# Performance work log

Hardware: AMD Instinct MI355X
Metric: run time of the kernel (lower is better)

Reference implementation:

```python
import jax, jax.numpy as jnp
import numpy as np

N_E = 1024     # codebook size (n_e, nbooks=1)
E_DIM = 256    # embedding dim
BETA = 0.25
B, T = 16, 4096


def setup_inputs() -> dict:
    key = jax.random.key(0)
    k1, k2 = jax.random.split(key)
    z = jax.random.normal(k1, (B, T, E_DIM), dtype=jnp.float32)
    # matches torch init: uniform(-1/n_e_i, 1/n_e_i)
    codebook = jax.random.uniform(k2, (N_E, E_DIM), dtype=jnp.float32,
                                  minval=-1.0 / N_E, maxval=1.0 / N_E)
    return {"z": z, "codebook": codebook}


def reference(z, codebook):
    zf = z.reshape(-1, E_DIM)                                   # [N, d]
    dist = (jnp.sum(zf * zf, axis=1, keepdims=True)
            - 2.0 * (zf @ codebook.T)
            + jnp.sum(codebook * codebook, axis=1)[None, :])
    idx = jnp.argmin(dist, axis=1)                              # [N]
    # one-hot scatter + matmul == codebook gather
    z_q = codebook[idx].reshape(z.shape)                        # [B, T, d]
    loss = (jnp.mean((z_q - jax.lax.stop_gradient(z)) ** 2)
            + BETA * jnp.mean((z - jax.lax.stop_gradient(z_q)) ** 2))
    # straight-through estimator
    z_q_st = z + jax.lax.stop_gradient(z_q - z)
    indices = idx.reshape(z.shape[:-1] + (1,))                  # [B, T, 1]
    return z_q_st, loss, indices
```

## Files before the change

kernel.cpp:

```cpp
#include <hip/hip_runtime.h>
#include <hip/hip_bf16.h>
#include <math.h>

typedef __bf16 bf16x8 __attribute__((ext_vector_type(8)));
typedef float f32x4 __attribute__((ext_vector_type(4)));
typedef unsigned short u16x8 __attribute__((ext_vector_type(8)));

constexpr int EDIM = 256;
constexpr int NE = 1024;
constexpr int NROWS = 65536;
constexpr float BETA = 0.25f;

constexpr size_t B2T_OFF   = 0;
constexpr size_t B2T_SZ    = (size_t)8 * 16 * 8192;
constexpr size_t SZROW_OFF = B2T_OFF + B2T_SZ;
constexpr size_t SZABS_OFF = SZROW_OFF + 262144;
constexpr size_t CNORM_OFF = SZABS_OFF + 262144;
constexpr size_t EMAX_OFF  = CNORM_OFF + 4096;
constexpr size_t CNT_OFF   = EMAX_OFF + 256;
constexpr size_t LIST_OFF  = CNT_OFF + 256;
constexpr size_t LPART_OFF = LIST_OFF + 262144;
constexpr size_t LP2_OFF   = LPART_OFF + 262144;
constexpr size_t WS_NEED   = LP2_OFF + 1024;

__device__ __forceinline__ unsigned short f32_to_bf16_rne(float f) {
    unsigned u = __float_as_uint(f);
    u += 0x7fffu + ((u >> 16) & 1u);
    return (unsigned short)(u >> 16);
}
__device__ __forceinline__ float bf16_to_f32(unsigned short h) {
    return __uint_as_float((unsigned)h << 16);
}

#define GLL16(g, l)                                                                   \
    __builtin_amdgcn_global_load_lds(                                                 \
        (const __attribute__((address_space(1))) unsigned int*)(g),                   \
        (__attribute__((address_space(3))) unsigned int*)(l), 16, 0, 0)

__global__ __launch_bounds__(64)
void p3_codebook(const float* __restrict__ cb, float* __restrict__ cnorm,
                 char* __restrict__ B2t, unsigned* __restrict__ emax_u) {
    __shared__ float xr[256];
    __shared__ float rres[16];
    __shared__ unsigned short ehi[256], elo[256];
    const int e = blockIdx.x, l = threadIdx.x;
    const float4 v = reinterpret_cast<const float4*>(cb + (size_t)e * EDIM)[l];
    *reinterpret_cast<float4*>(&xr[l * 4]) = v;
    float amax = fmaxf(fmaxf(fabsf(v.x), fabsf(v.y)), fmaxf(fabsf(v.z), fabsf(v.w)));
    #pragma unroll
    for (int off = 32; off; off >>= 1) amax = fmaxf(amax, __shfl_down(amax, off));
    __syncthreads();
    #pragma unroll
    for (int i = 0; i < 4; ++i) {
        const int idx = i * 64 + l;
        const float f = xr[idx];
        const unsigned short h = f32_to_bf16_rne(f);
        ehi[idx] = h;
        elo[idx] = f32_to_bf16_rne(f - bf16_to_f32(h));
    }
    if (l < 16) {
        const float* x = xr + (l >> 3) * 128;
        const int j = l & 7;
        float r = __fmul_rn(x[j], x[j]);
        for (int i = 8; i < 128; i += 8) r = __fadd_rn(r, __fmul_rn(x[i + j], x[i + j]));
        rres[l] = r;
    }
    __syncthreads();
    if (l == 0) {
        float h0 = __fadd_rn(__fadd_rn(__fadd_rn(rres[0], rres[1]), __fadd_rn(rres[2], rres[3])),
                             __fadd_rn(__fadd_rn(rres[4], rres[5]), __fadd_rn(rres[6], rres[7])));
        float h1 = __fadd_rn(__fadd_rn(__fadd_rn(rres[8], rres[9]), __fadd_rn(rres[10], rres[11])),
                             __fadd_rn(__fadd_rn(rres[12], rres[13]), __fadd_rn(rres[14], rres[15])));
        cnorm[e] = __fadd_rn(h0, h1);
        atomicMax(emax_u, __float_as_uint(amax));
    }
    {
        const int c = l >> 2, kgv = l & 3;
        const int colbase = ((c < 8) ? c * 32 : (c - 8) * 32) + kgv * 8;
        const unsigned short* src = (c < 8) ? ehi : elo;
        char* dst = B2t + ((((size_t)(e >> 7) * 16 + c) * 512 + (size_t)kgv * 128 + (e & 127)) * 16);
        *reinterpret_cast<uint4*>(dst) = *reinterpret_cast<const uint4*>(&src[colbase]);
    }
}

__global__ __launch_bounds__(256, 2)
void vq_main(const float* __restrict__ z, const char* __restrict__ B2t,
             const float* __restrict__ cnorm, const float* __restrict__ emaxp,
             const float* __restrict__ cb,
             float* __restrict__ idxf, int* __restrict__ cnt, int* __restrict__ list,
             float* __restrict__ zq, float* __restrict__ lpart,
             float* __restrict__ szrow, float* __restrict__ szabs) {
    constexpr int CNS = 65536;
    __shared__ char smem[71680] __attribute__((aligned(16)));
    float* cns  = reinterpret_cast<float*>(smem + CNS);
    float* szsr = reinterpret_cast<float*>(smem + 70656);
    float* szsa = reinterpret_cast<float*>(smem + 70912);
    float (*ms1)[2] = reinterpret_cast<float(*)[2]>(smem);
    float (*ms2)[2] = reinterpret_cast<float(*)[2]>(smem + 512);
    int   (*mi1)[2] = reinterpret_cast<int(*)[2]>(smem + 1024);
    int*  bidx      = reinterpret_cast<int*>(smem + 1536);

    const int tid = threadIdx.x;
    const int mtile = blockIdx.x;
    const size_t rowbase = (size_t)mtile * 64;
    const int l = tid & 63, wid = tid >> 6;
    const int kg = l >> 4, li = l & 15;
    const int wr = wid >> 1, wc = wid & 1;

    {
        float* t = reinterpret_cast<float*>(smem);
        #pragma unroll
        for (int i = 0; i < 16; ++i) {
            const int fid = i * 256 + tid;
            const int r = fid >> 6, c4 = fid & 63;
            const float4 v = *reinterpret_cast<const float4*>(
                z + (rowbase + r) * EDIM + c4 * 4);
            *reinterpret_cast<float4*>(&t[r * 260 + c4 * 4]) = v;
        }
    }
    __syncthreads();
    {
        float* t = reinterpret_cast<float*>(smem);
        float (*ch)[16] = reinterpret_cast<float(*)[16]>(smem + 66560);
        const int r = tid >> 2, q = tid & 3;
        float asum = 0.f;
        for (int c = 0; c < 64; ++c) asum += fabsf(t[r * 260 + q * 64 + c]);
        asum += __shfl_xor(asum, 1);
        asum += __shfl_xor(asum, 2);
        #pragma unroll
        for (int cc = 0; cc < 4; ++cc) {
            const int chain = q * 4 + cc;
            const float* x = &t[r * 260 + (chain >> 3) * 128];
            const int j = chain & 7;
            float rr = __fmul_rn(x[j], x[j]);
            for (int i = 8; i < 128; i += 8) rr = __fadd_rn(rr, __fmul_rn(x[i + j], x[i + j]));
            ch[r][chain] = rr;
        }
        __syncthreads();
        if (q == 0) {
            const float* c0 = ch[r];
            const float h0 = __fadd_rn(__fadd_rn(__fadd_rn(c0[0], c0[1]), __fadd_rn(c0[2], c0[3])),
                                       __fadd_rn(__fadd_rn(c0[4], c0[5]), __fadd_rn(c0[6], c0[7])));
            const float h1 = __fadd_rn(__fadd_rn(__fadd_rn(c0[8], c0[9]), __fadd_rn(c0[10], c0[11])),
                                       __fadd_rn(__fadd_rn(c0[12], c0[13]), __fadd_rn(c0[14], c0[15])));
            const float sz = __fadd_rn(h0, h1);
            szsr[r] = sz; szsa[r] = asum;
            szrow[rowbase + r] = sz;
            szabs[rowbase + r] = asum;
        }
    }
    u16x8 chi[8], clo[8];
    {
        float* t = reinterpret_cast<float*>(smem);
        const int r = tid >> 2, q = tid & 3;
        #pragma unroll
        for (int s = 0; s < 8; ++s) {
            u16x8 h, lw;
            #pragma unroll
            for (int j = 0; j < 8; ++j) {
                const float f = t[r * 260 + q * 64 + s * 8 + j];
                const unsigned short hh = f32_to_bf16_rne(f);
                h[j] = hh;
                lw[j] = f32_to_bf16_rne(f - bf16_to_f32(hh));
            }
            chi[s] = h; clo[s] = lw;
        }
    }
    __syncthreads();
    {
        const int r = tid >> 2, q = tid & 3;
        #pragma unroll
        for (int s = 0; s < 8; ++s) {
            const int ca = 2 * q + (s >> 2), kgv = s & 3;
            *reinterpret_cast<u16x8*>(smem + (ca * 256 + kgv * 64 + r) * 16) = chi[s];
            *reinterpret_cast<u16x8*>(smem + ((8 + ca) * 256 + kgv * 64 + r) * 16) = clo[s];
        }
    }
    GLL16((const char*)cnorm + tid * 16, smem + CNS + tid * 16);
    asm volatile("s_waitcnt vmcnt(0)" ::: "memory");
    __syncthreads();

    int aoff[2], boff[4];
    #pragma unroll
    for (int f = 0; f < 2; ++f)
        aoff[f] = kg * 1024 + (wr * 32 + f * 16 + li) * 16;
    #pragma unroll
    for (int f = 0; f < 4; ++f)
        boff[f] = kg * 2048 + (wc * 64 + f * 16 + li) * 16;

    bf16x8 cAh[2], cAl[2], cB[4];
    #pragma unroll
    for (int f = 0; f < 2; ++f) {
        cAh[f] = *reinterpret_cast<const bf16x8*>(smem + 0 * 4096 + aoff[f]);
        cAl[f] = *reinterpret_cast<const bf16x8*>(smem + 8 * 4096 + aoff[f]);
    }
    #pragma unroll
    for (int f = 0; f < 4; ++f)
        cB[f] = *reinterpret_cast<const bf16x8*>(B2t + boff[f]);

    float s1v[2][4], s2v[2][4];
    int i1v[2][4];
    #pragma unroll
    for (int a = 0; a < 2; ++a)
        #pragma unroll
        for (int b = 0; b < 4; ++b) { s1v[a][b] = 3.4e38f; s2v[a][b] = 3.4e38f; i1v[a][b] = 0; }

    for (int nt = 0; nt < 8; ++nt) {
        f32x4 acc[2][4];
        const f32x4 zf4 = {0.f, 0.f, 0.f, 0.f};
        #pragma unroll
        for (int a = 0; a < 2; ++a)
            #pragma unroll
            for (int b = 0; b < 4; ++b) acc[a][b] = zf4;

        #pragma unroll
        for (int j = 0; j < 16; ++j) {
            const int g = nt * 16 + j;
            bf16x8 nAh[2], nAl[2], nB[4];
            {
                const int jn = (j + 1) & 15;
                const char* gB = B2t + (size_t)(g + 1) * 8192;
                #pragma unroll
                for (int f = 0; f < 4; ++f)
                    nB[f] = *reinterpret_cast<const bf16x8*>(gB + boff[f]);
                if (jn < 8) {
                    #pragma unroll
                    for (int f = 0; f < 2; ++f) {
                        nAh[f] = *reinterpret_cast<const bf16x8*>(smem + jn * 4096 + aoff[f]);
                        nAl[f] = *reinterpret_cast<const bf16x8*>(smem + (8 + jn) * 4096 + aoff[f]);
                    }
                } else {
                    #pragma unroll
                    for (int f = 0; f < 2; ++f) {
                        nAh[f] = *reinterpret_cast<const bf16x8*>(smem + (jn - 8) * 4096 + aoff[f]);
                        nAl[f] = cAl[f];
                    }
                }
            }
            #pragma unroll
            for (int fm = 0; fm < 2; ++fm)
                #pragma unroll
                for (int fn = 0; fn < 4; ++fn)
                    acc[fm][fn] = __builtin_amdgcn_mfma_f32_16x16x32_bf16(cAh[fm], cB[fn], acc[fm][fn], 0, 0, 0);
            if (j < 8) {
                #pragma unroll
                for (int fm = 0; fm < 2; ++fm)
                    #pragma unroll
                    for (int fn = 0; fn < 4; ++fn)
                        acc[fm][fn] = __builtin_amdgcn_mfma_f32_16x16x32_bf16(cAl[fm], cB[fn], acc[fm][fn], 0, 0, 0);
            }
            #pragma unroll
            for (int f = 0; f < 2; ++f) { cAh[f] = nAh[f]; cAl[f] = nAl[f]; }
            #pragma unroll
            for (int f = 0; f < 4; ++f) cB[f] = nB[f];
        }

        const int ntb = nt * 128;
        #pragma unroll
        for (int fn = 0; fn < 4; ++fn) {
            const int e = ntb + wc * 64 + fn * 16 + li;
            const float cn = cns[e];
            #pragma unroll
            for (int fm = 0; fm < 2; ++fm)
                #pragma unroll
                for (int r = 0; r < 4; ++r) {
                    const float s = cn - 2.0f * acc[fm][fn][r];
                    if (s < s1v[fm][r]) { s2v[fm][r] = s1v[fm][r]; s1v[fm][r] = s; i1v[fm][r] = e; }
                    else s2v[fm][r] = fminf(s2v[fm][r], s);
                }
        }
    }

    __syncthreads();

    #pragma unroll
    for (int fm = 0; fm < 2; ++fm)
        #pragma unroll
        for (int r = 0; r < 4; ++r) {
            float s1 = s1v[fm][r], s2 = s2v[fm][r];
            int i1 = i1v[fm][r];
            #pragma unroll
            for (int off = 1; off < 16; off <<= 1) {
                const float os1 = __shfl_xor(s1, off);
                const float os2 = __shfl_xor(s2, off);
                const int oi1 = __shfl_xor(i1, off);
                const bool take = (os1 < s1) || (os1 == s1 && oi1 < i1);
                const float loser = take ? s1 : os1;
                if (take) { s1 = os1; i1 = oi1; }
                s2 = fminf(fminf(s2, os2), loser);
            }
            if (li == 0) {
                const int rloc = wr * 32 + fm * 16 + (kg << 2) + r;
                ms1[rloc][wc] = s1; ms2[rloc][wc] = s2; mi1[rloc][wc] = i1;
            }
        }
    __syncthreads();

    if (tid < 64) {
        const float a1 = ms1[tid][0], b1 = ms1[tid][1];
        const float a2 = ms2[tid][0], b2 = ms2[tid][1];
        const int ai = mi1[tid][0], bi = mi1[tid][1];
        const bool take = (b1 < a1) || (b1 == a1 && bi < ai);
        const float s1 = take ? b1 : a1;
        const int i1 = take ? bi : ai;
        const float loser = take ? a1 : b1;
        const float s2 = fminf(fminf(a2, b2), loser);
        const int rowg = (int)rowbase + tid;
        const float szv = szsr[tid], sab = szsa[tid];
        const float M = 2.0e-4f * sab * emaxp[0] + ldexpf(1.0f, ilogbf(szv * 1.02f) - 23);
        idxf[rowg] = (float)i1;
        lpart[rowg] = s1 + szv;
        bidx[tid] = i1;
        if (s2 - s1 <= 2.0f * M) { const int p = atomicAdd(cnt, 1); list[p] = rowg; }
    }
    __syncthreads();

    {
        const float4* cb4 = reinterpret_cast<const float4*>(cb);
        float4* zq4 = reinterpret_cast<float4*>(zq);
        #pragma unroll 4
        for (int j = 0; j < 16; ++j) {
            const int rr = wid * 16 + j;
            const int e = bidx[rr];
            zq4[(rowbase + rr) * 64 + l] = cb4[(size_t)e * 64 + l];
        }
    }
}

__global__ __launch_bounds__(256)
void vq_rescan(const float* __restrict__ z, const float* __restrict__ cb,
               const float* __restrict__ cnorm, const float* __restrict__ szrow,
               const int* __restrict__ list, const int* __restrict__ cntp,
               float* __restrict__ idxf, float* __restrict__ zq, float* __restrict__ lpart) {
    __shared__ float zr[8][260];
    __shared__ float szs[8];
    __shared__ int rows_s[8];
    __shared__ float sred[256];
    __shared__ int ired[256];
    const int tid = threadIdx.x;
    const int n = cntp[0];
    const int groups = (n + 7) >> 3;
    for (int g = blockIdx.x; g < groups; g += gridDim.x) {
        if (tid < 8) {
            const int gi = g * 8 + tid;
            const int row = (gi < n) ? list[gi] : -1;
            rows_s[tid] = row;
            szs[tid] = (row >= 0) ? szrow[row] : 0.f;
        }
        __syncthreads();
        #pragma unroll
        for (int i = 0; i < 8; ++i) {
            const int sid = i * 256 + tid;
            const int rr = sid >> 8, k = sid & 255;
            if (rows_s[rr] >= 0) zr[rr][k] = z[(size_t)rows_s[rr] * EDIM + k];
        }
        __syncthreads();
        float bs[8];
        int bi[8];
        #pragma unroll
        for (int rr = 0; rr < 8; ++rr) { bs[rr] = 3.4e38f; bi[rr] = 0; }
        for (int q = 0; q < 4; ++q) {
            const int e = tid + q * 256;
            const float4* crow = reinterpret_cast<const float4*>(cb + (size_t)e * EDIM);
            float d[8];
            #pragma unroll
            for (int rr = 0; rr < 8; ++rr) d[rr] = 0.f;
            for (int k4 = 0; k4 < 64; ++k4) {
                const float4 c4 = crow[k4];
                #pragma unroll
                for (int rr = 0; rr < 8; ++rr) {
                    d[rr] = fmaf(zr[rr][k4 * 4 + 0], c4.x, d[rr]);
                    d[rr] = fmaf(zr[rr][k4 * 4 + 1], c4.y, d[rr]);
                    d[rr] = fmaf(zr[rr][k4 * 4 + 2], c4.z, d[rr]);
                    d[rr] = fmaf(zr[rr][k4 * 4 + 3], c4.w, d[rr]);
                }
            }
            const float cn = cnorm[e];
            #pragma unroll
            for (int rr = 0; rr < 8; ++rr) {
                const float b1 = __fadd_rn(szs[rr], __fmul_rn(-2.0f, d[rr]));
                const float s = __fadd_rn(b1, cn);
                if (s < bs[rr]) { bs[rr] = s; bi[rr] = e; }
            }
        }
        #pragma unroll
        for (int rr = 0; rr < 8; ++rr) {
            sred[tid] = bs[rr];
            ired[tid] = bi[rr];
            __syncthreads();
            for (int h = 128; h; h >>= 1) {
                if (tid < h) {
                    const float so = sred[tid + h];
                    const int io = ired[tid + h];
                    if (so < sred[tid] || (so == sred[tid] && io < ired[tid])) {
                        sred[tid] = so; ired[tid] = io;
                    }
                }
                __syncthreads();
            }
            if (rows_s[rr] >= 0) {
                const int best = ired[0];
                const int row = rows_s[rr];
                zq[(size_t)row * EDIM + tid] = cb[(size_t)best * EDIM + tid];
                if (tid == 0) { idxf[row] = (float)best; lpart[row] = sred[0]; }
            }
            __syncthreads();
        }
    }
}

__global__ void vq_loss1(const float* __restrict__ lpart, float* __restrict__ lp2) {
    __shared__ float red[256];
    const int t = threadIdx.x;
    red[t] = lpart[blockIdx.x * 256 + t];
    __syncthreads();
    for (int h = 128; h; h >>= 1) {
        if (t < h) red[t] += red[t + h];
        __syncthreads();
    }
    if (t == 0) lp2[blockIdx.x] = red[0];
}
__global__ void vq_loss2(const float* __restrict__ lp2, float* __restrict__ outloss) {
    __shared__ float red[256];
    const int t = threadIdx.x;
    red[t] = lp2[t];
    __syncthreads();
    for (int h = 128; h; h >>= 1) {
        if (t < h) red[t] += red[t + h];
        __syncthreads();
    }
    if (t == 0) outloss[0] = red[0] * ((1.0f + BETA) / 16777216.0f);
}

__device__ __forceinline__ float np_sum128_sq(const float* __restrict__ x) {
    float r[8];
    #pragma unroll
    for (int j = 0; j < 8; ++j) r[j] = __fmul_rn(x[j], x[j]);
    #pragma unroll
    for (int i = 8; i < 128; i += 8)
        #pragma unroll
        for (int j = 0; j < 8; ++j) r[j] = __fadd_rn(r[j], __fmul_rn(x[i + j], x[i + j]));
    return __fadd_rn(__fadd_rn(__fadd_rn(r[0], r[1]), __fadd_rn(r[2], r[3])),
                     __fadd_rn(__fadd_rn(r[4], r[5]), __fadd_rn(r[6], r[7])));
}
__global__ void fb_prep(const float* __restrict__ z, const float* __restrict__ cb,
                        float* __restrict__ szrow, float* __restrict__ cnorm) {
    int t = blockIdx.x * blockDim.x + threadIdx.x;
    if (t < NROWS) {
        const float* x = z + (size_t)t * EDIM;
        szrow[t] = __fadd_rn(np_sum128_sq(x), np_sum128_sq(x + 128));
    } else if (t < NROWS + NE) {
        const float* x = cb + (size_t)(t - NROWS) * EDIM;
        cnorm[t - NROWS] = __fadd_rn(np_sum128_sq(x), np_sum128_sq(x + 128));
    }
}
__global__ __launch_bounds__(256, 2)
void fb_vq(const float* __restrict__ z, const float* __restrict__ cb,
           const float* __restrict__ cnorm, const float* __restrict__ szrow,
           float* __restrict__ zq, float* __restrict__ idxf, float* __restrict__ lpart) {
    __shared__ float As[64 * 268];
    __shared__ float Bs[32 * 68];
    __shared__ int bidx[64];
    __shared__ float lred[4];
    const int tid = threadIdx.x;
    const int tx = tid & 15, ty = tid >> 4;
    const size_t rowbase = (size_t)blockIdx.x * 64;
    const float4* zg = reinterpret_cast<const float4*>(z + rowbase * EDIM);
    #pragma unroll
    for (int it = 0; it < 16; ++it) {
        int id = it * 256 + tid;
        int r = id >> 6, c4 = id & 63;
        float4 v = zg[id];
        *reinterpret_cast<float4*>(&As[r * 268 + c4 * 4]) = v;
    }
    float sz[4];
    #pragma unroll
    for (int m = 0; m < 4; ++m) sz[m] = szrow[rowbase + ty * 4 + m];
    float bestS[4]; int bestI[4];
    #pragma unroll
    for (int m = 0; m < 4; ++m) { bestS[m] = 3.4e38f; bestI[m] = 0; }
    for (int nt = 0; nt < NE / 64; ++nt) {
        float acc[4][4];
        #pragma unroll
        for (int m = 0; m < 4; ++m)
            #pragma unroll
            for (int n = 0; n < 4; ++n) acc[m][n] = 0.f;
        const int ebase = nt * 64;
        for (int k0 = 0; k0 < EDIM; k0 += 32) {
            __syncthreads();
            #pragma unroll
            for (int i = 0; i < 8; ++i) {
                int id = i * 256 + tid;
                int n = id >> 5, k = id & 31;
                Bs[k * 68 + n] = cb[(size_t)(ebase + n) * EDIM + k0 + k];
            }
            __syncthreads();
            #pragma unroll
            for (int kg2 = 0; kg2 < 32; kg2 += 4) {
                float4 a[4], b[4];
                #pragma unroll
                for (int m = 0; m < 4; ++m)
                    a[m] = *reinterpret_cast<const float4*>(&As[(ty * 4 + m) * 268 + k0 + kg2]);
                #pragma unroll
                for (int kk = 0; kk < 4; ++kk)
                    b[kk] = *reinterpret_cast<const float4*>(&Bs[(kg2 + kk) * 68 + tx * 4]);
                #pragma unroll
                for (int m = 0; m < 4; ++m) {
                    const float* av = reinterpret_cast<const float*>(&a[m]);
                    #pragma unroll
                    for (int kk = 0; kk < 4; ++kk) {
                        acc[m][0] = fmaf(av[kk], b[kk].x, acc[m][0]);
                        acc[m][1] = fmaf(av[kk], b[kk].y, acc[m][1]);
                        acc[m][2] = fmaf(av[kk], b[kk].z, acc[m][2]);
                        acc[m][3] = fmaf(av[kk], b[kk].w, acc[m][3]);
                    }
                }
            }
        }
        #pragma unroll
        for (int n = 0; n < 4; ++n) {
            int e = ebase + tx * 4 + n;
            float cn = cnorm[e];
            #pragma unroll
            for (int m = 0; m < 4; ++m) {
                float b1 = __fadd_rn(sz[m], __fmul_rn(-2.0f, acc[m][n]));
                float s = __fadd_rn(b1, cn);
                if (s < bestS[m]) { bestS[m] = s; bestI[m] = e; }
            }
        }
    }
    #pragma unroll
    for (int m = 0; m < 4; ++m) {
        float s = bestS[m]; int i = bestI[m];
        #pragma unroll
        for (int off = 1; off < 16; off <<= 1) {
            float s2 = __shfl_xor(s, off);
            int i2 = __shfl_xor(i, off);
            if (s2 < s || (s2 == s && i2 < i)) { s = s2; i = i2; }
        }
        if (tx == 0) bidx[ty * 4 + m] = i;
    }
    __syncthreads();
    if (tid < 64) idxf[rowbase + tid] = (float)bidx[tid];
    float lsum = 0.f;
    for (int r = 0; r < 64; ++r) {
        int e = bidx[r];
        float c = cb[(size_t)e * EDIM + tid];
        float zv = As[r * 268 + tid];
        float d = c - zv;
        lsum = fmaf(d, d, lsum);
        zq[(rowbase + r) * EDIM + tid] = c;
    }
    #pragma unroll
    for (int off = 32; off; off >>= 1) lsum += __shfl_down(lsum, off);
    if ((tid & 63) == 0) lred[tid >> 6] = lsum;
    __syncthreads();
    if (tid == 0) lpart[blockIdx.x] = lred[0] + lred[1] + lred[2] + lred[3];
}
__global__ void fb_loss(const float* __restrict__ lpart, float* __restrict__ out_loss) {
    __shared__ float red[256];
    int tid = threadIdx.x;
    float s = 0.f;
    for (int i = tid; i < NROWS / 64; i += 256) s += lpart[i];
    red[tid] = s;
    __syncthreads();
    for (int h = 128; h; h >>= 1) {
        if (tid < h) red[tid] += red[tid + h];
        __syncthreads();
    }
    if (tid == 0) out_loss[0] = red[0] * (1.0f + BETA) / (float)((size_t)NROWS * EDIM);
}

extern "C" void kernel_launch(void* const* d_in, const int* in_sizes, int n_in,
                              void* d_out, int out_size, void* d_ws, size_t ws_size,
                              hipStream_t stream) {
    const float* z = (const float*)d_in[0];
    const float* cb = (const float*)d_in[1];
    float* out = (float*)d_out;
    float* zq = out;
    float* loss = out + (size_t)NROWS * EDIM;
    float* idxf = loss + 1;
    char* ws = (char*)d_ws;

    if (ws_size < WS_NEED) {
        float* cnorm = (float*)ws;
        float* szrow = cnorm + NE;
        float* lpart = szrow + NROWS;
        hipLaunchKernelGGL(fb_prep, dim3((NROWS + NE + 255) / 256), dim3(256), 0, stream, z, cb, szrow, cnorm);
        hipLaunchKernelGGL(fb_vq, dim3(NROWS / 64), dim3(256), 0, stream, z, cb, cnorm, szrow, zq, idxf, lpart);
        hipLaunchKernelGGL(fb_loss, dim3(1), dim3(256), 0, stream, lpart, loss);
        return;
    }

    char* B2t = ws + B2T_OFF;
    float* szrow = (float*)(ws + SZROW_OFF);
    float* szabs = (float*)(ws + SZABS_OFF);
    float* cnorm = (float*)(ws + CNORM_OFF);
    float* emax = (float*)(ws + EMAX_OFF);
    int* cnt = (int*)(ws + CNT_OFF);
    int* list = (int*)(ws + LIST_OFF);
    float* lpart = (float*)(ws + LPART_OFF);
    float* lp2 = (float*)(ws + LP2_OFF);

    hipMemsetAsync(emax, 0, 4, stream);
    hipMemsetAsync(cnt, 0, 4, stream);
    hipLaunchKernelGGL(p3_codebook, dim3(NE), dim3(64), 0, stream, cb, cnorm, B2t, (unsigned*)emax);
    hipLaunchKernelGGL(vq_main, dim3(1024), dim3(256), 0, stream,
                       z, B2t, cnorm, emax, cb, idxf, cnt, list, zq, lpart, szrow, szabs);
    hipLaunchKernelGGL(vq_rescan, dim3(1024), dim3(256), 0, stream,
                       z, cb, cnorm, szrow, list, cnt, idxf, zq, lpart);
    hipLaunchKernelGGL(vq_loss1, dim3(256), dim3(256), 0, stream, lpart, lp2);
    hipLaunchKernelGGL(vq_loss2, dim3(1), dim3(256), 0, stream, lp2, loss);
}
```

Measured before the change: 237.5 us.

## Shrink vq_main tile to 32 rows for higher occupancy

Halves the per-block row tile from 64 to 32 rows, so shared memory drops from about 70KB to about 37KB and launch bounds rise to 4 blocks per CU. The grid doubles to 2048 blocks and the four waves now split the 128-code N tile as 1x4 instead of 2x2, with a 4-way cross-wave argmin merge. The goal is more resident waves to hide latency, at the cost of each block streaming the whole bf16 codebook for only half as many rows, which doubles codebook traffic per row.

```diff
diff --git a/kernel.cpp b/kernel.cpp
--- a/kernel.cpp
+++ b/kernel.cpp
@@ -83,34 +83,34 @@
     }
 }
 
-__global__ __launch_bounds__(256, 2)
+__global__ __launch_bounds__(256, 4)
 void vq_main(const float* __restrict__ z, const char* __restrict__ B2t,
              const float* __restrict__ cnorm, const float* __restrict__ emaxp,
              const float* __restrict__ cb,
              float* __restrict__ idxf, int* __restrict__ cnt, int* __restrict__ list,
              float* __restrict__ zq, float* __restrict__ lpart,
              float* __restrict__ szrow, float* __restrict__ szabs) {
-    constexpr int CNS = 65536;
-    __shared__ char smem[71680] __attribute__((aligned(16)));
+    constexpr int CNS = 32768;
+    __shared__ char smem[37120] __attribute__((aligned(16)));
     float* cns  = reinterpret_cast<float*>(smem + CNS);
-    float* szsr = reinterpret_cast<float*>(smem + 70656);
-    float* szsa = reinterpret_cast<float*>(smem + 70912);
-    float (*ms1)[2] = reinterpret_cast<float(*)[2]>(smem);
-    float (*ms2)[2] = reinterpret_cast<float(*)[2]>(smem + 512);
-    int   (*mi1)[2] = reinterpret_cast<int(*)[2]>(smem + 1024);
+    float* szsr = reinterpret_cast<float*>(smem + 36864);
+    float* szsa = reinterpret_cast<float*>(smem + 36992);
+    float (*ms1)[4] = reinterpret_cast<float(*)[4]>(smem);
+    float (*ms2)[4] = reinterpret_cast<float(*)[4]>(smem + 512);
+    int   (*mi1)[4] = reinterpret_cast<int(*)[4]>(smem + 1024);
     int*  bidx      = reinterpret_cast<int*>(smem + 1536);
 
     const int tid = threadIdx.x;
     const int mtile = blockIdx.x;
-    const size_t rowbase = (size_t)mtile * 64;
+    const size_t rowbase = (size_t)mtile * 32;
     const int l = tid & 63, wid = tid >> 6;
     const int kg = l >> 4, li = l & 15;
-    const int wr = wid >> 1, wc = wid & 1;
+    const int wc = wid;
 
     {
         float* t = reinterpret_cast<float*>(smem);
         #pragma unroll
-        for (int i = 0; i < 16; ++i) {
+        for (int i = 0; i < 8; ++i) {
             const int fid = i * 256 + tid;
             const int r = fid >> 6, c4 = fid & 63;
             const float4 v = *reinterpret_cast<const float4*>(
@@ -121,15 +121,16 @@
     __syncthreads();
     {
         float* t = reinterpret_cast<float*>(smem);
-        float (*ch)[16] = reinterpret_cast<float(*)[16]>(smem + 66560);
-        const int r = tid >> 2, q = tid & 3;
+        float (*ch)[16] = reinterpret_cast<float(*)[16]>(smem + 33280);
+        const int r = tid >> 3, q = tid & 7;
         float asum = 0.f;
-        for (int c = 0; c < 64; ++c) asum += fabsf(t[r * 260 + q * 64 + c]);
+        for (int c = 0; c < 32; ++c) asum += fabsf(t[r * 260 + q * 32 + c]);
         asum += __shfl_xor(asum, 1);
         asum += __shfl_xor(asum, 2);
-        #pragma unroll
-        for (int cc = 0; cc < 4; ++cc) {
-            const int chain = q * 4 + cc;
+        asum += __shfl_xor(asum, 4);
+        #pragma unroll
+        for (int cc = 0; cc < 2; ++cc) {
+            const int chain = q * 2 + cc;
             const float* x = &t[r * 260 + (chain >> 3) * 128];
             const int j = chain & 7;
             float rr = __fmul_rn(x[j], x[j]);
@@ -149,16 +150,16 @@
             szabs[rowbase + r] = asum;
         }
     }
-    u16x8 chi[8], clo[8];
+    u16x8 chi[4], clo[4];
     {
         float* t = reinterpret_cast<float*>(smem);
-        const int r = tid >> 2, q = tid & 3;
-        #pragma unroll
-        for (int s = 0; s < 8; ++s) {
+        const int r = tid >> 3, q = tid & 7;
+        #pragma unroll
+        for (int s = 0; s < 4; ++s) {
             u16x8 h, lw;
             #pragma unroll
             for (int j = 0; j < 8; ++j) {
-                const float f = t[r * 260 + q * 64 + s * 8 + j];
+                const float f = t[r * 260 + q * 32 + s * 8 + j];
                 const unsigned short hh = f32_to_bf16_rne(f);
                 h[j] = hh;
                 lw[j] = f32_to_bf16_rne(f - bf16_to_f32(hh));
@@ -168,35 +169,31 @@
     }
     __syncthreads();
     {
-        const int r = tid >> 2, q = tid & 3;
-        #pragma unroll
-        for (int s = 0; s < 8; ++s) {
-            const int ca = 2 * q + (s >> 2), kgv = s & 3;
-            *reinterpret_cast<u16x8*>(smem + (ca * 256 + kgv * 64 + r) * 16) = chi[s];
-            *reinterpret_cast<u16x8*>(smem + ((8 + ca) * 256 + kgv * 64 + r) * 16) = clo[s];
+        const int r = tid >> 3, q = tid & 7;
+        #pragma unroll
+        for (int s = 0; s < 4; ++s) {
+            *reinterpret_cast<u16x8*>(smem + (q * 128 + s * 32 + r) * 16) = chi[s];
+            *reinterpret_cast<u16x8*>(smem + ((8 + q) * 128 + s * 32 + r) * 16) = clo[s];
         }
     }
     GLL16((const char*)cnorm + tid * 16, smem + CNS + tid * 16);
     asm volatile("s_waitcnt vmcnt(0)" ::: "memory");
     __syncthreads();
 
-    int aoff[2], boff[4];
-    #pragma unroll
-    for (int f = 0; f < 2; ++f)
-        aoff[f] = kg * 1024 + (wr * 32 + f * 16 + li) * 16;
-    #pragma unroll
-    for (int f = 0; f < 4; ++f)
-        boff[f] = kg * 2048 + (wc * 64 + f * 16 + li) * 16;
-
-    bf16x8 cAh[2], cAl[2], cB[4];
+    int aoff[2], boff[2];
     #pragma unroll
     for (int f = 0; f < 2; ++f) {
-        cAh[f] = *reinterpret_cast<const bf16x8*>(smem + 0 * 4096 + aoff[f]);
-        cAl[f] = *reinterpret_cast<const bf16x8*>(smem + 8 * 4096 + aoff[f]);
-    }
-    #pragma unroll
-    for (int f = 0; f < 4; ++f)
-        cB[f] = *reinterpret_cast<const bf16x8*>(B2t + boff[f]);
+        aoff[f] = kg * 512 + (f * 16 + li) * 16;
+        boff[f] = kg * 2048 + (wc * 32 + f * 16 + li) * 16;
+    }
+
+    bf16x8 cAh[2], cAl[2], cB[2];
+    #pragma unroll
+    for (int f = 0; f < 2; ++f) {
+        cAh[f] = *reinterpret_cast<const bf16x8*>(smem + 0 * 2048 + aoff[f]);
+        cAl[f] = *reinterpret_cast<const bf16x8*>(smem + 8 * 2048 + aoff[f]);
+        cB[f]  = *reinterpret_cast<const bf16x8*>(B2t + boff[f]);
+    }
 
     float s1v[2][4], s2v[2][4];
     int i1v[2][4];
@@ -206,33 +203,33 @@
         for (int b = 0; b < 4; ++b) { s1v[a][b] = 3.4e38f; s2v[a][b] = 3.4e38f; i1v[a][b] = 0; }
 
     for (int nt = 0; nt < 8; ++nt) {
-        f32x4 acc[2][4];
+        f32x4 acc[2][2];
         const f32x4 zf4 = {0.f, 0.f, 0.f, 0.f};
         #pragma unroll
         for (int a = 0; a < 2; ++a)
             #pragma unroll
-            for (int b = 0; b < 4; ++b) acc[a][b] = zf4;
+            for (int b = 0; b < 2; ++b) acc[a][b] = zf4;
 
         #pragma unroll
         for (int j = 0; j < 16; ++j) {
             const int g = nt * 16 + j;
-            bf16x8 nAh[2], nAl[2], nB[4];
+            bf16x8 nAh[2], nAl[2], nB[2];
             {
                 const int jn = (j + 1) & 15;
                 const char* gB = B2t + (size_t)(g + 1) * 8192;
                 #pragma unroll
-                for (int f = 0; f < 4; ++f)
+                for (int f = 0; f < 2; ++f)
                     nB[f] = *reinterpret_cast<const bf16x8*>(gB + boff[f]);
                 if (jn < 8) {
                     #pragma unroll
                     for (int f = 0; f < 2; ++f) {
-                        nAh[f] = *reinterpret_cast<const bf16x8*>(smem + jn * 4096 + aoff[f]);
-                        nAl[f] = *reinterpret_cast<const bf16x8*>(smem + (8 + jn) * 4096 + aoff[f]);
+                        nAh[f] = *reinterpret_cast<const bf16x8*>(smem + jn * 2048 + aoff[f]);
+                        nAl[f] = *reinterpret_cast<const bf16x8*>(smem + (8 + jn) * 2048 + aoff[f]);
                     }
                 } else {
                     #pragma unroll
                     for (int f = 0; f < 2; ++f) {
-                        nAh[f] = *reinterpret_cast<const bf16x8*>(smem + (jn - 8) * 4096 + aoff[f]);
+                        nAh[f] = *reinterpret_cast<const bf16x8*>(smem + (jn - 8) * 2048 + aoff[f]);
                         nAl[f] = cAl[f];
                     }
                 }
@@ -240,25 +237,23 @@
             #pragma unroll
             for (int fm = 0; fm < 2; ++fm)
                 #pragma unroll
-                for (int fn = 0; fn < 4; ++fn)
+                for (int fn = 0; fn < 2; ++fn)
                     acc[fm][fn] = __builtin_amdgcn_mfma_f32_16x16x32_bf16(cAh[fm], cB[fn], acc[fm][fn], 0, 0, 0);
             if (j < 8) {
                 #pragma unroll
                 for (int fm = 0; fm < 2; ++fm)
                     #pragma unroll
-                    for (int fn = 0; fn < 4; ++fn)
+                    for (int fn = 0; fn < 2; ++fn)
                         acc[fm][fn] = __builtin_amdgcn_mfma_f32_16x16x32_bf16(cAl[fm], cB[fn], acc[fm][fn], 0, 0, 0);
             }
             #pragma unroll
-            for (int f = 0; f < 2; ++f) { cAh[f] = nAh[f]; cAl[f] = nAl[f]; }
-            #pragma unroll
-            for (int f = 0; f < 4; ++f) cB[f] = nB[f];
+            for (int f = 0; f < 2; ++f) { cAh[f] = nAh[f]; cAl[f] = nAl[f]; cB[f] = nB[f]; }
         }
 
         const int ntb = nt * 128;
         #pragma unroll
-        for (int fn = 0; fn < 4; ++fn) {
-            const int e = ntb + wc * 64 + fn * 16 + li;
+        for (int fn = 0; fn < 2; ++fn) {
+            const int e = ntb + wc * 32 + fn * 16 + li;
             const float cn = cns[e];
             #pragma unroll
             for (int fm = 0; fm < 2; ++fm)
@@ -290,21 +285,24 @@
                 s2 = fminf(fminf(s2, os2), loser);
             }
             if (li == 0) {
-                const int rloc = wr * 32 + fm * 16 + (kg << 2) + r;
+                const int rloc = fm * 16 + (kg << 2) + r;
                 ms1[rloc][wc] = s1; ms2[rloc][wc] = s2; mi1[rloc][wc] = i1;
             }
         }
     __syncthreads();
 
-    if (tid < 64) {
-        const float a1 = ms1[tid][0], b1 = ms1[tid][1];
-        const float a2 = ms2[tid][0], b2 = ms2[tid][1];
-        const int ai = mi1[tid][0], bi = mi1[tid][1];
-        const bool take = (b1 < a1) || (b1 == a1 && bi < ai);
-        const float s1 = take ? b1 : a1;
-        const int i1 = take ? bi : ai;
-        const float loser = take ? a1 : b1;
-        const float s2 = fminf(fminf(a2, b2), loser);
+    if (tid < 32) {
+        float s1 = ms1[tid][0], s2 = ms2[tid][0];
+        int i1 = mi1[tid][0];
+        #pragma unroll
+        for (int q = 1; q < 4; ++q) {
+            const float o1 = ms1[tid][q], o2 = ms2[tid][q];
+            const int oi = mi1[tid][q];
+            const bool take = (o1 < s1) || (o1 == s1 && oi < i1);
+            const float loser = take ? s1 : o1;
+            if (take) { s1 = o1; i1 = oi; }
+            s2 = fminf(fminf(s2, o2), loser);
+        }
         const int rowg = (int)rowbase + tid;
         const float szv = szsr[tid], sab = szsa[tid];
         const float M = 2.0e-4f * sab * emaxp[0] + ldexpf(1.0f, ilogbf(szv * 1.02f) - 23);
@@ -319,8 +317,8 @@
         const float4* cb4 = reinterpret_cast<const float4*>(cb);
         float4* zq4 = reinterpret_cast<float4*>(zq);
         #pragma unroll 4
-        for (int j = 0; j < 16; ++j) {
-            const int rr = wid * 16 + j;
+        for (int j = 0; j < 8; ++j) {
+            const int rr = wid * 8 + j;
             const int e = bidx[rr];
             zq4[(rowbase + rr) * 64 + l] = cb4[(size_t)e * 64 + l];
         }
@@ -605,7 +603,7 @@
     hipMemsetAsync(emax, 0, 4, stream);
     hipMemsetAsync(cnt, 0, 4, stream);
     hipLaunchKernelGGL(p3_codebook, dim3(NE), dim3(64), 0, stream, cb, cnorm, B2t, (unsigned*)emax);
-    hipLaunchKernelGGL(vq_main, dim3(1024), dim3(256), 0, stream,
+    hipLaunchKernelGGL(vq_main, dim3(2048), dim3(256), 0, stream,
                        z, B2t, cnorm, emax, cb, idxf, cnt, list, zq, lpart, szrow, szabs);
     hipLaunchKernelGGL(vq_rescan, dim3(1024), dim3(256), 0, stream,
                        z, cb, cnorm, szrow, list, cnt, idxf, zq, lpart);
```

Measured after the change: 355.5 us. +49.7%, slower.
